# Kernel optimization log

Measured on AMD Instinct MI355X. Metric: run time of the kernel, lower is better.

Reference implementation:

```python
import jax, jax.numpy as jnp
import numpy as np

N_NODES = 50000
N_EDGES = 150000
D_FEAT = 512
HIDDEN = 512
N_CLASSES = 47


def gcn_conv(x, edge_index, W, b, n_nodes):
    """PyG GCNConv: out = D^{-1/2} (A + I) D^{-1/2} (x @ W) + b."""
    h = x @ W  # [N, out_dim] dense GEMM
    loop = jnp.arange(n_nodes, dtype=edge_index.dtype)
    row = jnp.concatenate([edge_index[0], loop])  # source
    col = jnp.concatenate([edge_index[1], loop])  # target
    ones = jnp.ones(row.shape[0], dtype=h.dtype)
    deg = jax.ops.segment_sum(ones, col, num_segments=n_nodes)  # in-degree + 1
    dinv = jnp.where(deg > 0, jax.lax.rsqrt(deg), 0.0)
    norm = dinv[row] * dinv[col]  # [E+N]
    msg = norm[:, None] * h[row]  # gather + scale
    out = jax.ops.segment_sum(msg, col, num_segments=n_nodes)  # scatter-add
    return out + b


def setup_inputs() -> dict:
    key = jax.random.key(0)
    k1, k2, k3, k4, k5, k6 = jax.random.split(key, 6)
    x = jax.random.normal(k1, (N_NODES, D_FEAT), dtype=jnp.float32)
    edge_index = jax.random.randint(k2, (2, N_EDGES), 0, N_NODES, dtype=jnp.int64)
    s1 = (6.0 / (D_FEAT + HIDDEN)) ** 0.5
    s2 = (6.0 / (HIDDEN + N_CLASSES)) ** 0.5
    W1 = jax.random.uniform(k3, (D_FEAT, HIDDEN), jnp.float32, -s1, s1)
    b1 = jnp.zeros((HIDDEN,), jnp.float32)
    W2 = jax.random.uniform(k4, (HIDDEN, N_CLASSES), jnp.float32, -s2, s2)
    b2 = jnp.zeros((N_CLASSES,), jnp.float32)
    return {"x": x, "edge_index": edge_index, "W1": W1, "b1": b1, "W2": W2, "b2": b2}


def reference(x, edge_index, W1, b1, W2, b2):
    n = x.shape[0]
    h = gcn_conv(x, edge_index, W1, b1, n)
    h = jax.nn.relu(h)
    # F.dropout(p=0.5, training=self.training): eval mode -> identity
    out = gcn_conv(h, edge_index, W2, b2, n)
    return out
```

## Files before the change

### kernel.cpp

```cpp
#include <hip/hip_runtime.h>
#include <hip/hip_bf16.h>

#define NNODES 50000
#define NEDGES 150000
#define DFEAT  512
#define HID    512
#define NCLS   47

typedef __hip_bfloat16 bf16;
typedef __attribute__((ext_vector_type(8))) short short8;
typedef __attribute__((ext_vector_type(4))) float float4v;

typedef const __attribute__((address_space(1))) unsigned int* gas_t;
typedef __attribute__((address_space(3))) unsigned int* las_t;
__device__ __forceinline__ void load_lds16(const void* g, void* l) {
    __builtin_amdgcn_global_load_lds((gas_t)g, (las_t)l, 16, 0, 0);
}

__device__ __forceinline__ float bfbits_lo(unsigned int w) {
    return __uint_as_float((w & 0xFFFFu) << 16);
}
__device__ __forceinline__ float bfbits_hi(unsigned int w) {
    return __uint_as_float(w & 0xFFFF0000u);
}

__global__ void k_detect(const void* x, const void* ei, int* flags) {
    __shared__ int scnt[64], sor[64];
    int t = threadIdx.x;
    const unsigned short* xs = (const unsigned short*)x;
    int c = 0;
    for (int i = t; i < 256; i += 64) {
        unsigned int e = (xs[2 * i] >> 7) & 0xFF;
        c += (e >= 117 && e <= 130) ? 1 : 0;
    }
    const int* w = (const int*)ei;
    int o = 0;
    for (int i = 2 * t + 1; i < 512; i += 128) o |= w[i];
    scnt[t] = c; sor[t] = o;
    __syncthreads();
    if (t == 0) {
        int C = 0, O = 0;
        for (int i = 0; i < 64; i++) { C += scnt[i]; O |= sor[i]; }
        flags[0] = (C > 128) ? 1 : 0;
        flags[1] = (O == 0) ? 1 : 0;
    }
}

__device__ __forceinline__ int eidx(const void* ei, int half, int e, int is64) {
    if (is64) return (int)((const long long*)ei)[(size_t)half * NEDGES + e];
    return ((const int*)ei)[half * NEDGES + e];
}

__global__ void k_zero32(unsigned int* p, size_t n) {
    size_t i = (size_t)blockIdx.x * blockDim.x + threadIdx.x;
    if (i < n) p[i] = 0u;
}

__global__ void k_cvt(const void* src, float* dst, int n, const int* flags) {
    int i = blockIdx.x * blockDim.x + threadIdx.x;
    if (i >= n) return;
    dst[i] = flags[0] ? __bfloat162float(((const bf16*)src)[i]) : ((const float*)src)[i];
}

__global__ void k_cvt_w1t(const void* W1, bf16* W1T, const int* flags) {
    int i = blockIdx.x * blockDim.x + threadIdx.x;
    if (i >= DFEAT * HID) return;
    int k = i / HID, n = i % HID;
    float v = flags[0] ? __bfloat162float(((const bf16*)W1)[i]) : ((const float*)W1)[i];
    W1T[(size_t)n * DFEAT + k] = __float2bfloat16(v);
}

__global__ void k_cvt_w2t(const void* W2, bf16* W2T, const int* flags) {
    int i = blockIdx.x * blockDim.x + threadIdx.x;
    if (i >= 64 * HID) return;
    int n = i / HID, k = i % HID;
    float v = 0.0f;
    if (n < NCLS) {
        size_t idx = (size_t)k * NCLS + n;
        v = flags[0] ? __bfloat162float(((const bf16*)W2)[idx]) : ((const float*)W2)[idx];
    }
    W2T[(size_t)n * HID + k] = __float2bfloat16(v);
}

__global__ void k_count(const void* ei, int* cnt, const int* flags) {
    int e = blockIdx.x * blockDim.x + threadIdx.x;
    if (e >= NEDGES) return;
    atomicAdd(&cnt[eidx(ei, 1, e, flags[1])], 1);
}

__global__ void k_dinv(const int* cnt, float* dinv) {
    int i = blockIdx.x * blockDim.x + threadIdx.x;
    if (i < NNODES) dinv[i] = rsqrtf(1.0f + (float)cnt[i]);
}

__global__ __launch_bounds__(256) void k_scan_part(const int* cnt, int* part) {
    __shared__ int s[256];
    int i = blockIdx.x * 256 + threadIdx.x;
    s[threadIdx.x] = (i < NNODES) ? cnt[i] : 0;
    __syncthreads();
    for (int off = 128; off > 0; off >>= 1) {
        if (threadIdx.x < off) s[threadIdx.x] += s[threadIdx.x + off];
        __syncthreads();
    }
    if (threadIdx.x == 0) part[blockIdx.x] = s[0];
}

__global__ __launch_bounds__(256) void k_scan_off(int* part, int n) {
    __shared__ int s[256];
    int v = (threadIdx.x < n) ? part[threadIdx.x] : 0;
    s[threadIdx.x] = v;
    __syncthreads();
    for (int off = 1; off < 256; off <<= 1) {
        int t = (threadIdx.x >= off) ? s[threadIdx.x - off] : 0;
        __syncthreads();
        s[threadIdx.x] += t;
        __syncthreads();
    }
    if (threadIdx.x < n) part[threadIdx.x] = s[threadIdx.x] - v;
}

__global__ __launch_bounds__(256) void k_scan_fin(const int* cnt, const int* part,
                                                  int* rowptr, int* cursor) {
    __shared__ int s[256];
    int i = blockIdx.x * 256 + threadIdx.x;
    int v = (i < NNODES) ? cnt[i] : 0;
    s[threadIdx.x] = v;
    __syncthreads();
    for (int off = 1; off < 256; off <<= 1) {
        int t = (threadIdx.x >= off) ? s[threadIdx.x - off] : 0;
        __syncthreads();
        s[threadIdx.x] += t;
        __syncthreads();
    }
    int incl = s[threadIdx.x] + part[blockIdx.x];
    if (i < NNODES) {
        rowptr[i + 1] = incl;
        cursor[i] = incl - v;
    }
    if (i == 0) rowptr[0] = 0;
}

__global__ void k_fill(const void* ei, int* cursor, int* csr_src, const int* flags) {
    int e = blockIdx.x * blockDim.x + threadIdx.x;
    if (e >= NEDGES) return;
    int is64 = flags[1];
    int v = eidx(ei, 1, e, is64);
    int u = eidx(ei, 0, e, is64);
    int pos = atomicAdd(&cursor[v], 1);
    csr_src[pos] = u;
}

__global__ __launch_bounds__(256, 2) void k_gemm1_v4(
    const void* __restrict__ X, const bf16* __restrict__ W1T,
    bf16* __restrict__ h1c, int c0, int C, const int* __restrict__ flags,
    int col_tiles, int rows_per_xcd, int n_row_tiles) {
    const int b = blockIdx.x;
    const int xcd = b & 7;
    const int s = b >> 3;
    const int col_t = s % col_tiles;
    const int lr = s / col_tiles;
    const int row_t = xcd * rows_per_xcd + lr;
    if (row_t >= n_row_tiles) return;

    __shared__ bf16 As[2][128 * 64];
    __shared__ bf16 Bs[2][128 * 64];
    const int tid = threadIdx.x;
    const int wave = tid >> 6, lane = tid & 63;
    const int row0 = row_t * 128;
    const int gc0 = c0 + col_t * 128;
    const int isb = flags[0];

    float4v acc[2][8];
#pragma unroll
    for (int i = 0; i < 2; i++)
#pragma unroll
        for (int j = 0; j < 8; j++) acc[i][j] = (float4v){0.f, 0.f, 0.f, 0.f};

    const int rb = wave * 32;
    const int frow = lane & 15;
    const int fk = lane >> 4;

    auto stageAB = [&](int k0, bf16* Asb, bf16* Bsb) {
        if (isb) {
            const bf16* xb = (const bf16*)X;
#pragma unroll
            for (int t = 0; t < 4; ++t) {
                int g8 = wave * 4 + t;
                int r = g8 * 8 + (lane >> 3);
                int gr = row0 + r; if (gr >= NNODES) gr = NNODES - 1;
                int ck = (lane & 7) ^ (r & 7);
                load_lds16(xb + (size_t)gr * DFEAT + k0 + ck * 8, Asb + g8 * 8 * 64);
            }
        } else {
            const float* xf = (const float*)X;
            for (int i = tid; i < 128 * 8; i += 256) {
                int r = i >> 3, p = i & 7;
                int gr = row0 + r; if (gr >= NNODES) gr = NNODES - 1;
                int ck = p ^ (r & 7);
                const float* src = xf + (size_t)gr * DFEAT + k0 + ck * 8;
#pragma unroll
                for (int e = 0; e < 8; ++e)
                    Asb[r * 64 + p * 8 + e] = __float2bfloat16(src[e]);
            }
        }
#pragma unroll
        for (int t = 0; t < 4; ++t) {
            int g8 = wave * 4 + t;
            int cl = g8 * 8 + (lane >> 3);
            int ck = (lane & 7) ^ (cl & 7);
            load_lds16(W1T + (size_t)(gc0 + cl) * DFEAT + k0 + ck * 8, Bsb + g8 * 8 * 64);
        }
    };

    stageAB(0, As[0], Bs[0]);
    __syncthreads();
    int cur = 0;

    for (int k0 = 0; k0 < DFEAT; k0 += 64) {
        if (k0 + 64 < DFEAT) stageAB(k0 + 64, As[cur ^ 1], Bs[cur ^ 1]);
        const bf16* Ac = As[cur];
        const bf16* Bc = Bs[cur];
#pragma unroll
        for (int ki = 0; ki < 2; ++ki) {
            const int cc = ki * 4 + fk;
            short8 a[2], b8[8];
#pragma unroll
            for (int i = 0; i < 2; i++) {
                int r = rb + i * 16 + frow;
                a[i] = *(const short8*)&Ac[r * 64 + (cc ^ (r & 7)) * 8];
            }
#pragma unroll
            for (int j = 0; j < 8; j++) {
                int cl = j * 16 + frow;
                b8[j] = *(const short8*)&Bc[cl * 64 + (cc ^ (cl & 7)) * 8];
            }
#pragma unroll
            for (int i = 0; i < 2; i++)
#pragma unroll
                for (int j = 0; j < 8; j++)
                    acc[i][j] = __builtin_amdgcn_mfma_f32_16x16x32_bf16(a[i], b8[j], acc[i][j], 0, 0, 0);
        }
        __syncthreads();
        cur ^= 1;
    }

    const int ccol = gc0 - c0;
#pragma unroll
    for (int i = 0; i < 2; i++) {
#pragma unroll
        for (int r = 0; r < 4; r++) {
            int grow = row0 + rb + i * 16 + (lane >> 4) * 4 + r;
            if (grow < NNODES) {
#pragma unroll
                for (int j = 0; j < 8; j++)
                    h1c[(size_t)grow * C + ccol + j * 16 + (lane & 15)] =
                        __float2bfloat16(acc[i][j][r]);
            }
        }
    }
}

__global__ __launch_bounds__(256) void k_gemm1_mfma(
    const void* __restrict__ X, const bf16* __restrict__ W1T,
    bf16* __restrict__ h1c, int c0, int C, const int* __restrict__ flags) {
    __shared__ bf16 As[128 * 64];
    __shared__ bf16 Bs[64 * 64];
    const int tid = threadIdx.x;
    const int wave = tid >> 6, lane = tid & 63;
    const int row0 = blockIdx.x * 128;
    const int gc0 = c0 + blockIdx.y * 64;
    const int isb = flags[0];
    float4v acc[2][4];
#pragma unroll
    for (int i = 0; i < 2; i++)
#pragma unroll
        for (int j = 0; j < 4; j++) acc[i][j] = (float4v){0.f, 0.f, 0.f, 0.f};
    const int rbase = wave * 32;
    const int fl_row = lane & 15;
    const int fl_k8 = (lane >> 4) * 8;
    for (int k0 = 0; k0 < DFEAT; k0 += 64) {
        __syncthreads();
        if (isb) {
            const bf16* xb = (const bf16*)X;
#pragma unroll
            for (int i = 0; i < 4; ++i) {
                int r = i * 32 + wave * 8;
                int gr = row0 + r + (lane >> 3);
                if (gr >= NNODES) gr = NNODES - 1;
                load_lds16(xb + (size_t)gr * DFEAT + k0 + (lane & 7) * 8, &As[r * 64]);
            }
        } else {
            const float* xf = (const float*)X;
            for (int i = tid; i < 128 * 64; i += 256) {
                int r = i >> 6, c = i & 63;
                int gr = row0 + r;
                if (gr >= NNODES) gr = NNODES - 1;
                As[i] = __float2bfloat16(xf[(size_t)gr * DFEAT + k0 + c]);
            }
        }
#pragma unroll
        for (int i = 0; i < 2; ++i) {
            int r = i * 32 + wave * 8;
            int gn = gc0 + r + (lane >> 3);
            load_lds16(W1T + (size_t)gn * DFEAT + k0 + (lane & 7) * 8, &Bs[r * 64]);
        }
        __syncthreads();
#pragma unroll
        for (int ki = 0; ki < 64; ki += 32) {
            short8 a[2], b[4];
#pragma unroll
            for (int i = 0; i < 2; i++)
                a[i] = *(const short8*)&As[(rbase + i * 16 + fl_row) * 64 + ki + fl_k8];
#pragma unroll
            for (int j = 0; j < 4; j++)
                b[j] = *(const short8*)&Bs[(j * 16 + fl_row) * 64 + ki + fl_k8];
#pragma unroll
            for (int i = 0; i < 2; i++)
#pragma unroll
                for (int j = 0; j < 4; j++)
                    acc[i][j] = __builtin_amdgcn_mfma_f32_16x16x32_bf16(a[i], b[j], acc[i][j], 0, 0, 0);
        }
    }
    const int ccol = blockIdx.y * 64;
#pragma unroll
    for (int i = 0; i < 2; i++) {
#pragma unroll
        for (int r = 0; r < 4; r++) {
            int grow = row0 + rbase + i * 16 + (lane >> 4) * 4 + r;
            if (grow < NNODES) {
#pragma unroll
                for (int j = 0; j < 4; j++)
                    h1c[(size_t)grow * C + ccol + j * 16 + (lane & 15)] =
                        __float2bfloat16(acc[i][j][r]);
            }
        }
    }
}

__global__ __launch_bounds__(256) void k_agg1_512(const bf16* __restrict__ h1c,
                                                  const int* __restrict__ rowptr,
                                                  const int* __restrict__ csr_src,
                                                  const float* __restrict__ dinv,
                                                  const float* __restrict__ b1c,
                                                  bf16* __restrict__ a1c) {
    int v = blockIdx.x * 4 + (threadIdx.x >> 6);
    int lane = threadIdx.x & 63;
    if (v >= NNODES) return;
    int d8 = lane * 8;
    float dv = dinv[v];
    float s2 = dv * dv;
    uint4 w = *(const uint4*)(h1c + (size_t)v * 512 + d8);
    float a0 = s2 * bfbits_lo(w.x), a1 = s2 * bfbits_hi(w.x);
    float a2 = s2 * bfbits_lo(w.y), a3 = s2 * bfbits_hi(w.y);
    float a4 = s2 * bfbits_lo(w.z), a5 = s2 * bfbits_hi(w.z);
    float a6 = s2 * bfbits_lo(w.w), a7 = s2 * bfbits_hi(w.w);
    int pend = rowptr[v + 1];
    for (int p = rowptr[v]; p < pend; ++p) {
        int u = csr_src[p];
        float nw = dinv[u] * dv;
        uint4 q = *(const uint4*)(h1c + (size_t)u * 512 + d8);
        a0 += nw * bfbits_lo(q.x); a1 += nw * bfbits_hi(q.x);
        a2 += nw * bfbits_lo(q.y); a3 += nw * bfbits_hi(q.y);
        a4 += nw * bfbits_lo(q.z); a5 += nw * bfbits_hi(q.z);
        a6 += nw * bfbits_lo(q.w); a7 += nw * bfbits_hi(q.w);
    }
    const float* bb = b1c + d8;
    a0 += bb[0]; a1 += bb[1]; a2 += bb[2]; a3 += bb[3];
    a4 += bb[4]; a5 += bb[5]; a6 += bb[6]; a7 += bb[7];
    bf16 o[8];
    o[0] = __float2bfloat16(a0 > 0.f ? a0 : 0.f);
    o[1] = __float2bfloat16(a1 > 0.f ? a1 : 0.f);
    o[2] = __float2bfloat16(a2 > 0.f ? a2 : 0.f);
    o[3] = __float2bfloat16(a3 > 0.f ? a3 : 0.f);
    o[4] = __float2bfloat16(a4 > 0.f ? a4 : 0.f);
    o[5] = __float2bfloat16(a5 > 0.f ? a5 : 0.f);
    o[6] = __float2bfloat16(a6 > 0.f ? a6 : 0.f);
    o[7] = __float2bfloat16(a7 > 0.f ? a7 : 0.f);
    *(uint4*)(a1c + (size_t)v * 512 + d8) = *(uint4*)o;
}

__global__ __launch_bounds__(256) void k_agg1(const bf16* __restrict__ h1c,
                                              const int* __restrict__ rowptr,
                                              const int* __restrict__ csr_src,
                                              const float* __restrict__ dinv,
                                              const float* __restrict__ b1c, int c0, int C,
                                              bf16* __restrict__ a1c) {
    const int tshift = (C == 512) ? 7 : (C == 256) ? 6 : (C == 128) ? 5 : 4;
    long long gt = (long long)blockIdx.x * 256 + threadIdx.x;
    int v = (int)(gt >> tshift);
    int d4 = (int)((gt & ((1 << tshift) - 1)) << 2);
    if (v >= NNODES) return;
    float dv = dinv[v];
    uint2 w = *(const uint2*)(h1c + (size_t)v * C + d4);
    float s2 = dv * dv;
    float a0 = s2 * bfbits_lo(w.x), a1 = s2 * bfbits_hi(w.x);
    float a2 = s2 * bfbits_lo(w.y), a3 = s2 * bfbits_hi(w.y);
    int pend = rowptr[v + 1];
    for (int p = rowptr[v]; p < pend; ++p) {
        int u = csr_src[p];
        float nw = dinv[u] * dv;
        uint2 q = *(const uint2*)(h1c + (size_t)u * C + d4);
        a0 += nw * bfbits_lo(q.x); a1 += nw * bfbits_hi(q.x);
        a2 += nw * bfbits_lo(q.y); a3 += nw * bfbits_hi(q.y);
    }
    const float* bb = b1c + c0 + d4;
    a0 += bb[0]; a1 += bb[1]; a2 += bb[2]; a3 += bb[3];
    bf16 o[4];
    o[0] = __float2bfloat16(a0 > 0.f ? a0 : 0.f);
    o[1] = __float2bfloat16(a1 > 0.f ? a1 : 0.f);
    o[2] = __float2bfloat16(a2 > 0.f ? a2 : 0.f);
    o[3] = __float2bfloat16(a3 > 0.f ? a3 : 0.f);
    *(uint2*)(a1c + (size_t)v * C + d4) = *(uint2*)o;
}

__global__ __launch_bounds__(256, 3) void k_gemm2_v2(
    const bf16* __restrict__ A, int C, const bf16* __restrict__ W2T, int kg0,
    float* __restrict__ h2, int accum) {
    __shared__ bf16 As[2][128 * 64];
    __shared__ bf16 Bs[2][64 * 64];
    const int tid = threadIdx.x;
    const int wave = tid >> 6, lane = tid & 63;
    const int row0 = blockIdx.x * 128;
    float4v acc[2][4];
#pragma unroll
    for (int i = 0; i < 2; i++)
#pragma unroll
        for (int j = 0; j < 4; j++) acc[i][j] = (float4v){0.f, 0.f, 0.f, 0.f};
    const int rb = wave * 32;
    const int frow = lane & 15;
    const int fk = lane >> 4;

    auto stage2 = [&](int kk, bf16* Asb, bf16* Bsb) {
#pragma unroll
        for (int t = 0; t < 4; ++t) {
            int g8 = wave * 4 + t;
            int r = g8 * 8 + (lane >> 3);
            int gr = row0 + r; if (gr >= NNODES) gr = NNODES - 1;
            int ck = (lane & 7) ^ (r & 7);
            load_lds16(A + (size_t)gr * C + kk + ck * 8, Asb + g8 * 8 * 64);
        }
#pragma unroll
        for (int t = 0; t < 2; ++t) {
            int g8 = wave * 2 + t;
            int cl = g8 * 8 + (lane >> 3);
            int ck = (lane & 7) ^ (cl & 7);
            load_lds16(W2T + (size_t)cl * HID + kg0 + kk + ck * 8, Bsb + g8 * 8 * 64);
        }
    };

    stage2(0, As[0], Bs[0]);
    __syncthreads();
    int cur = 0;

    for (int kk = 0; kk < C; kk += 64) {
        if (kk + 64 < C) stage2(kk + 64, As[cur ^ 1], Bs[cur ^ 1]);
        const bf16* Ac = As[cur];
        const bf16* Bc = Bs[cur];
#pragma unroll
        for (int ki = 0; ki < 2; ++ki) {
            const int cc = ki * 4 + fk;
            short8 a[2], b8[4];
#pragma unroll
            for (int i = 0; i < 2; i++) {
                int r = rb + i * 16 + frow;
                a[i] = *(const short8*)&Ac[r * 64 + (cc ^ (r & 7)) * 8];
            }
#pragma unroll
            for (int j = 0; j < 4; j++) {
                int cl = j * 16 + frow;
                b8[j] = *(const short8*)&Bc[cl * 64 + (cc ^ (cl & 7)) * 8];
            }
#pragma unroll
            for (int i = 0; i < 2; i++)
#pragma unroll
                for (int j = 0; j < 4; j++)
                    acc[i][j] = __builtin_amdgcn_mfma_f32_16x16x32_bf16(a[i], b8[j], acc[i][j], 0, 0, 0);
        }
        __syncthreads();
        cur ^= 1;
    }
#pragma unroll
    for (int i = 0; i < 2; i++) {
#pragma unroll
        for (int r = 0; r < 4; r++) {
            int grow = row0 + rb + i * 16 + (lane >> 4) * 4 + r;
            if (grow < NNODES) {
#pragma unroll
                for (int j = 0; j < 4; j++) {
                    int col = j * 16 + (lane & 15);
                    if (col < NCLS) {
                        size_t o = (size_t)grow * NCLS + col;
                        h2[o] = accum ? h2[o] + acc[i][j][r] : acc[i][j][r];
                    }
                }
            }
        }
    }
}

__global__ __launch_bounds__(256) void k_agg2(const float* __restrict__ h2,
                                              const int* __restrict__ rowptr,
                                              const int* __restrict__ csr_src,
                                              const float* __restrict__ dinv,
                                              const float* __restrict__ b2c,
                                              void* out, const int* flags) {
    int v = blockIdx.x * 4 + (threadIdx.x >> 6);
    int d = threadIdx.x & 63;
    if (v >= NNODES || d >= NCLS) return;
    float dv = dinv[v];
    float acc = dv * dv * h2[(size_t)v * NCLS + d];
    int pend = rowptr[v + 1];
    for (int p = rowptr[v]; p < pend; ++p) {
        int u = csr_src[p];
        acc += dinv[u] * dv * h2[(size_t)u * NCLS + d];
    }
    acc += b2c[d];
    size_t o = (size_t)v * NCLS + d;
    if (flags[0]) ((bf16*)out)[o] = __float2bfloat16(acc);
    else          ((float*)out)[o] = acc;
}

extern "C" void kernel_launch(void* const* d_in, const int* in_sizes, int n_in,
                              void* d_out, int out_size, void* d_ws, size_t ws_size,
                              hipStream_t stream) {
    const void* x  = d_in[0];
    const void* ei = d_in[1];
    const void* W1 = d_in[2];
    const void* b1 = d_in[3];
    const void* W2 = d_in[4];
    const void* b2 = d_in[5];

    char* base = (char*)d_ws;
    auto alloc = [&](size_t bytes) -> char* {
        char* p = base;
        base += (bytes + 255) & ~(size_t)255;
        return p;
    };
    int*   flags  = (int*)alloc(64);
    int*   cnt    = (int*)alloc(sizeof(int) * NNODES);
    int*   part   = (int*)alloc(sizeof(int) * 256);
    int*   rowptr = (int*)alloc(sizeof(int) * (NNODES + 1));
    int*   cursor = (int*)alloc(sizeof(int) * NNODES);
    int*   csr    = (int*)alloc(sizeof(int) * NEDGES);
    float* dinv   = (float*)alloc(sizeof(float) * NNODES);
    bf16*  W1T    = (bf16*)alloc(sizeof(bf16) * DFEAT * HID);
    float* b1c    = (float*)alloc(sizeof(float) * HID);
    bf16*  W2T    = (bf16*)alloc(sizeof(bf16) * 64 * HID);
    float* b2c    = (float*)alloc(sizeof(float) * 64);
    float* h2     = (float*)alloc(sizeof(float) * (size_t)NNODES * NCLS);

    size_t used = (size_t)(base - (char*)d_ws);
    size_t rem = (ws_size > used) ? ws_size - used : 0;
    int C = 64;
    if (rem >= (size_t)200000 * 512 + 1024) C = 512;
    else if (rem >= (size_t)200000 * 256 + 1024) C = 256;
    else if (rem >= (size_t)200000 * 128 + 1024) C = 128;
    bf16* h1c = (bf16*)alloc(sizeof(bf16) * (size_t)NNODES * C);
    bf16* a1c = (bf16*)alloc(sizeof(bf16) * (size_t)NNODES * C);

    k_detect<<<1, 64, 0, stream>>>(x, ei, flags);
    k_zero32<<<(NNODES + 255) / 256, 256, 0, stream>>>((unsigned int*)cnt, NNODES);

    k_cvt_w1t<<<(DFEAT * HID + 255) / 256, 256, 0, stream>>>(W1, W1T, flags);
    k_cvt<<<(HID + 255) / 256, 256, 0, stream>>>(b1, b1c, HID, flags);
    k_cvt_w2t<<<(64 * HID + 255) / 256, 256, 0, stream>>>(W2, W2T, flags);
    k_cvt<<<1, 64, 0, stream>>>(b2, b2c, NCLS, flags);

    k_count<<<(NEDGES + 255) / 256, 256, 0, stream>>>(ei, cnt, flags);
    k_dinv<<<(NNODES + 255) / 256, 256, 0, stream>>>(cnt, dinv);
    const int nsb = (NNODES + 255) / 256;
    k_scan_part<<<nsb, 256, 0, stream>>>(cnt, part);
    k_scan_off<<<1, 256, 0, stream>>>(part, nsb);
    k_scan_fin<<<nsb, 256, 0, stream>>>(cnt, part, rowptr, cursor);
    k_fill<<<(NEDGES + 255) / 256, 256, 0, stream>>>(ei, cursor, csr, flags);

    const int rowblocks = (NNODES + 127) / 128;
    const int rows_per_xcd = (rowblocks + 7) / 8;
    int chunk_i = 0;
    for (int c0 = 0; c0 < HID; c0 += C, ++chunk_i) {
        if (C >= 128) {
            int col_tiles = C / 128;
            int nblk = 8 * rows_per_xcd * col_tiles;
            k_gemm1_v4<<<nblk, 256, 0, stream>>>(x, W1T, h1c, c0, C, flags,
                                                 col_tiles, rows_per_xcd, rowblocks);
        } else {
            dim3 g1(rowblocks, 1);
            k_gemm1_mfma<<<g1, 256, 0, stream>>>(x, W1T, h1c, c0, C, flags);
        }
        if (C == 512) {
            k_agg1_512<<<(NNODES + 3) / 4, 256, 0, stream>>>(h1c, rowptr, csr, dinv, b1c, a1c);
        } else {
            size_t nthr = (size_t)NNODES * (C / 4);
            k_agg1<<<(int)((nthr + 255) / 256), 256, 0, stream>>>(h1c, rowptr, csr, dinv, b1c, c0, C, a1c);
        }
        k_gemm2_v2<<<rowblocks, 256, 0, stream>>>(a1c, C, W2T, c0, h2, chunk_i > 0 ? 1 : 0);
    }

    k_agg2<<<(NNODES + 3) / 4, 256, 0, stream>>>(h2, rowptr, csr, dinv, b2c, d_out, flags);
}
```

Before: 370.8 us.

## Rewrite GEMM1 with per-wave triple-buffered A staging and direct-register B loads

The first-layer GEMM now uses 128x64 tiles in which each wave stages only its own 32 rows of X into a private triple-buffered LDS region and waits on vmcnt instead of block-wide barriers. W1T fragments are read straight from global memory into registers rather than staged through LDS, which frees LDS and registers so occupancy can be raised to 3 blocks per SIMD. This removes __syncthreads stalls and B-tile LDS traffic, at the cost of redundant global reads of W1T across waves and a narrower column tile that re-reads X more often. The old fallback kernel for small chunk sizes is removed.

```diff
diff --git a/kernel.cpp b/kernel.cpp
--- a/kernel.cpp
+++ b/kernel.cpp
@@ -150,7 +150,7 @@
     csr_src[pos] = u;
 }
 
-__global__ __launch_bounds__(256, 2) void k_gemm1_v4(
+__global__ __launch_bounds__(256, 3) void k_gemm1_v7(
     const void* __restrict__ X, const bf16* __restrict__ W1T,
     bf16* __restrict__ h1c, int c0, int C, const int* __restrict__ flags,
     int col_tiles, int rows_per_xcd, int n_row_tiles) {
@@ -162,89 +162,111 @@
     const int row_t = xcd * rows_per_xcd + lr;
     if (row_t >= n_row_tiles) return;
 
-    __shared__ bf16 As[2][128 * 64];
-    __shared__ bf16 Bs[2][128 * 64];
+    __shared__ bf16 As[4][3][32 * 64];
     const int tid = threadIdx.x;
     const int wave = tid >> 6, lane = tid & 63;
     const int row0 = row_t * 128;
-    const int gc0 = c0 + col_t * 128;
+    const int gc0 = c0 + col_t * 64;
     const int isb = flags[0];
-
-    float4v acc[2][8];
-#pragma unroll
-    for (int i = 0; i < 2; i++)
-#pragma unroll
-        for (int j = 0; j < 8; j++) acc[i][j] = (float4v){0.f, 0.f, 0.f, 0.f};
 
     const int rb = wave * 32;
     const int frow = lane & 15;
     const int fk = lane >> 4;
 
-    auto stageAB = [&](int k0, bf16* Asb, bf16* Bsb) {
-        if (isb) {
-            const bf16* xb = (const bf16*)X;
-#pragma unroll
-            for (int t = 0; t < 4; ++t) {
-                int g8 = wave * 4 + t;
-                int r = g8 * 8 + (lane >> 3);
-                int gr = row0 + r; if (gr >= NNODES) gr = NNODES - 1;
-                int ck = (lane & 7) ^ (r & 7);
-                load_lds16(xb + (size_t)gr * DFEAT + k0 + ck * 8, Asb + g8 * 8 * 64);
-            }
-        } else {
-            const float* xf = (const float*)X;
-            for (int i = tid; i < 128 * 8; i += 256) {
-                int r = i >> 3, p = i & 7;
-                int gr = row0 + r; if (gr >= NNODES) gr = NNODES - 1;
-                int ck = p ^ (r & 7);
-                const float* src = xf + (size_t)gr * DFEAT + k0 + ck * 8;
+    float4v acc[2][4];
+#pragma unroll
+    for (int i = 0; i < 2; i++)
+#pragma unroll
+        for (int j = 0; j < 4; j++) acc[i][j] = (float4v){0.f, 0.f, 0.f, 0.f};
+
+    auto stageA = [&](int k0, int bi) {
+        const bf16* xb = (const bf16*)X;
+        bf16* dst = &As[wave][bi][0];
+#pragma unroll
+        for (int t = 0; t < 4; ++t) {
+            int rl = t * 8 + (lane >> 3);
+            int gr = row0 + rb + rl; if (gr >= NNODES) gr = NNODES - 1;
+            int ck = (lane & 7) ^ (rl & 7);
+            load_lds16(xb + (size_t)gr * DFEAT + k0 + ck * 8, dst + t * 8 * 64);
+        }
+    };
+
+    if (isb) {
+        stageA(0, 0);
+        stageA(64, 1);
+#pragma unroll
+        for (int t = 0; t < 8; ++t) {
+            const int k0 = t * 64;
+            short8 b8[2][4];
+#pragma unroll
+            for (int ki = 0; ki < 2; ++ki)
+#pragma unroll
+                for (int j = 0; j < 4; ++j)
+                    b8[ki][j] = *(const short8*)(W1T +
+                        (size_t)(gc0 + j * 16 + frow) * DFEAT + k0 + ki * 32 + fk * 8);
+            __builtin_amdgcn_sched_barrier(0);
+            if (t + 2 < 8) stageA(k0 + 128, (t + 2) % 3);
+            __builtin_amdgcn_sched_barrier(0);
+            asm volatile("s_waitcnt vmcnt(16)" ::: "memory");
+            __builtin_amdgcn_sched_barrier(0);
+            const bf16* Ac = &As[wave][t % 3][0];
+#pragma unroll
+            for (int ki = 0; ki < 2; ++ki) {
+                const int cc = ki * 4 + fk;
+                short8 a[2];
+#pragma unroll
+                for (int i = 0; i < 2; i++) {
+                    int rl = i * 16 + frow;
+                    a[i] = *(const short8*)&Ac[rl * 64 + (cc ^ (rl & 7)) * 8];
+                }
+#pragma unroll
+                for (int i = 0; i < 2; i++)
+#pragma unroll
+                    for (int j = 0; j < 4; j++)
+                        acc[i][j] = __builtin_amdgcn_mfma_f32_16x16x32_bf16(a[i], b8[ki][j], acc[i][j], 0, 0, 0);
+            }
+        }
+    } else {
+        const float* xf = (const float*)X;
+        for (int t = 0; t < 8; ++t) {
+            const int k0 = t * 64;
+            bf16* dst = &As[wave][0][0];
+            int rl = lane >> 1;
+            int gr = row0 + rb + rl; if (gr >= NNODES) gr = NNODES - 1;
+#pragma unroll
+            for (int pp = 0; pp < 4; ++pp) {
+                int p = (lane & 1) * 4 + pp;
+                const float* src = xf + (size_t)gr * DFEAT + k0 + ((p ^ (rl & 7)) * 8);
 #pragma unroll
                 for (int e = 0; e < 8; ++e)
-                    Asb[r * 64 + p * 8 + e] = __float2bfloat16(src[e]);
-            }
-        }
-#pragma unroll
-        for (int t = 0; t < 4; ++t) {
-            int g8 = wave * 4 + t;
-            int cl = g8 * 8 + (lane >> 3);
-            int ck = (lane & 7) ^ (cl & 7);
-            load_lds16(W1T + (size_t)(gc0 + cl) * DFEAT + k0 + ck * 8, Bsb + g8 * 8 * 64);
-        }
-    };
-
-    stageAB(0, As[0], Bs[0]);
-    __syncthreads();
-    int cur = 0;
-
-    for (int k0 = 0; k0 < DFEAT; k0 += 64) {
-        if (k0 + 64 < DFEAT) stageAB(k0 + 64, As[cur ^ 1], Bs[cur ^ 1]);
-        const bf16* Ac = As[cur];
-        const bf16* Bc = Bs[cur];
-#pragma unroll
-        for (int ki = 0; ki < 2; ++ki) {
-            const int cc = ki * 4 + fk;
-            short8 a[2], b8[8];
-#pragma unroll
-            for (int i = 0; i < 2; i++) {
-                int r = rb + i * 16 + frow;
-                a[i] = *(const short8*)&Ac[r * 64 + (cc ^ (r & 7)) * 8];
-            }
-#pragma unroll
-            for (int j = 0; j < 8; j++) {
-                int cl = j * 16 + frow;
-                b8[j] = *(const short8*)&Bc[cl * 64 + (cc ^ (cl & 7)) * 8];
-            }
-#pragma unroll
-            for (int i = 0; i < 2; i++)
-#pragma unroll
-                for (int j = 0; j < 8; j++)
-                    acc[i][j] = __builtin_amdgcn_mfma_f32_16x16x32_bf16(a[i], b8[j], acc[i][j], 0, 0, 0);
-        }
-        __syncthreads();
-        cur ^= 1;
-    }
-
-    const int ccol = gc0 - c0;
+                    dst[rl * 64 + p * 8 + e] = __float2bfloat16(src[e]);
+            }
+            short8 b8[2][4];
+#pragma unroll
+            for (int ki = 0; ki < 2; ++ki)
+#pragma unroll
+                for (int j = 0; j < 4; ++j)
+                    b8[ki][j] = *(const short8*)(W1T +
+                        (size_t)(gc0 + j * 16 + frow) * DFEAT + k0 + ki * 32 + fk * 8);
+#pragma unroll
+            for (int ki = 0; ki < 2; ++ki) {
+                const int cc = ki * 4 + fk;
+                short8 a[2];
+#pragma unroll
+                for (int i = 0; i < 2; i++) {
+                    int rl2 = i * 16 + frow;
+                    a[i] = *(const short8*)&dst[rl2 * 64 + (cc ^ (rl2 & 7)) * 8];
+                }
+#pragma unroll
+                for (int i = 0; i < 2; i++)
+#pragma unroll
+                    for (int j = 0; j < 4; j++)
+                        acc[i][j] = __builtin_amdgcn_mfma_f32_16x16x32_bf16(a[i], b8[ki][j], acc[i][j], 0, 0, 0);
+            }
+        }
+    }
+
+    const int ccol0 = (gc0 - c0);
 #pragma unroll
     for (int i = 0; i < 2; i++) {
 #pragma unroll
@@ -252,85 +274,8 @@
             int grow = row0 + rb + i * 16 + (lane >> 4) * 4 + r;
             if (grow < NNODES) {
 #pragma unroll
-                for (int j = 0; j < 8; j++)
-                    h1c[(size_t)grow * C + ccol + j * 16 + (lane & 15)] =
-                        __float2bfloat16(acc[i][j][r]);
-            }
-        }
-    }
-}
-
-__global__ __launch_bounds__(256) void k_gemm1_mfma(
-    const void* __restrict__ X, const bf16* __restrict__ W1T,
-    bf16* __restrict__ h1c, int c0, int C, const int* __restrict__ flags) {
-    __shared__ bf16 As[128 * 64];
-    __shared__ bf16 Bs[64 * 64];
-    const int tid = threadIdx.x;
-    const int wave = tid >> 6, lane = tid & 63;
-    const int row0 = blockIdx.x * 128;
-    const int gc0 = c0 + blockIdx.y * 64;
-    const int isb = flags[0];
-    float4v acc[2][4];
-#pragma unroll
-    for (int i = 0; i < 2; i++)
-#pragma unroll
-        for (int j = 0; j < 4; j++) acc[i][j] = (float4v){0.f, 0.f, 0.f, 0.f};
-    const int rbase = wave * 32;
-    const int fl_row = lane & 15;
-    const int fl_k8 = (lane >> 4) * 8;
-    for (int k0 = 0; k0 < DFEAT; k0 += 64) {
-        __syncthreads();
-        if (isb) {
-            const bf16* xb = (const bf16*)X;
-#pragma unroll
-            for (int i = 0; i < 4; ++i) {
-                int r = i * 32 + wave * 8;
-                int gr = row0 + r + (lane >> 3);
-                if (gr >= NNODES) gr = NNODES - 1;
-                load_lds16(xb + (size_t)gr * DFEAT + k0 + (lane & 7) * 8, &As[r * 64]);
-            }
-        } else {
-            const float* xf = (const float*)X;
-            for (int i = tid; i < 128 * 64; i += 256) {
-                int r = i >> 6, c = i & 63;
-                int gr = row0 + r;
-                if (gr >= NNODES) gr = NNODES - 1;
-                As[i] = __float2bfloat16(xf[(size_t)gr * DFEAT + k0 + c]);
-            }
-        }
-#pragma unroll
-        for (int i = 0; i < 2; ++i) {
-            int r = i * 32 + wave * 8;
-            int gn = gc0 + r + (lane >> 3);
-            load_lds16(W1T + (size_t)gn * DFEAT + k0 + (lane & 7) * 8, &Bs[r * 64]);
-        }
-        __syncthreads();
-#pragma unroll
-        for (int ki = 0; ki < 64; ki += 32) {
-            short8 a[2], b[4];
-#pragma unroll
-            for (int i = 0; i < 2; i++)
-                a[i] = *(const short8*)&As[(rbase + i * 16 + fl_row) * 64 + ki + fl_k8];
-#pragma unroll
-            for (int j = 0; j < 4; j++)
-                b[j] = *(const short8*)&Bs[(j * 16 + fl_row) * 64 + ki + fl_k8];
-#pragma unroll
-            for (int i = 0; i < 2; i++)
-#pragma unroll
                 for (int j = 0; j < 4; j++)
-                    acc[i][j] = __builtin_amdgcn_mfma_f32_16x16x32_bf16(a[i], b[j], acc[i][j], 0, 0, 0);
-        }
-    }
-    const int ccol = blockIdx.y * 64;
-#pragma unroll
-    for (int i = 0; i < 2; i++) {
-#pragma unroll
-        for (int r = 0; r < 4; r++) {
-            int grow = row0 + rbase + i * 16 + (lane >> 4) * 4 + r;
-            if (grow < NNODES) {
-#pragma unroll
-                for (int j = 0; j < 4; j++)
-                    h1c[(size_t)grow * C + ccol + j * 16 + (lane & 15)] =
+                    h1c[(size_t)grow * C + ccol0 + j * 16 + frow] =
                         __float2bfloat16(acc[i][j][r]);
             }
         }
@@ -487,7 +432,7 @@
             if (grow < NNODES) {
 #pragma unroll
                 for (int j = 0; j < 4; j++) {
-                    int col = j * 16 + (lane & 15);
+                    int col = j * 16 + frow;
                     if (col < NCLS) {
                         size_t o = (size_t)grow * NCLS + col;
                         h2[o] = accum ? h2[o] + acc[i][j][r] : acc[i][j][r];
@@ -578,14 +523,11 @@
     const int rows_per_xcd = (rowblocks + 7) / 8;
     int chunk_i = 0;
     for (int c0 = 0; c0 < HID; c0 += C, ++chunk_i) {
-        if (C >= 128) {
-            int col_tiles = C / 128;
+        {
+            int col_tiles = C / 64;
             int nblk = 8 * rows_per_xcd * col_tiles;
-            k_gemm1_v4<<<nblk, 256, 0, stream>>>(x, W1T, h1c, c0, C, flags,
+            k_gemm1_v7<<<nblk, 256, 0, stream>>>(x, W1T, h1c, c0, C, flags,
                                                  col_tiles, rows_per_xcd, rowblocks);
-        } else {
-            dim3 g1(rowblocks, 1);
-            k_gemm1_mfma<<<g1, 256, 0, stream>>>(x, W1T, h1c, c0, C, flags);
         }
         if (C == 512) {
             k_agg1_512<<<(NNODES + 3) / 4, 256, 0, stream>>>(h1c, rowptr, csr, dinv, b1c, a1c);
```

Result: slower. 413.4 us (+11.5%).
